# Kernel optimization log

Hardware: AMD Instinct MI355X
Metric: run time of the kernel (lower is better)

## Reference

```python
import jax, jax.numpy as jnp
import numpy as np
from functools import partial

B, T, F = 4096, 256, 32
H1, H2, NT = 64, 32, 3


def _lstm_layer(x, W_ih, W_hh, b_ih, b_hh):
    """Torch-style LSTM (batch_first). x: [B,T,Fin], W_ih: [4H,Fin], W_hh: [4H,H].
    Gate order i, f, g, o. Returns all hidden states [B,T,H]."""
    Bsz = x.shape[0]
    H = W_hh.shape[1]
    # Precompute input contribution for all timesteps (one big GEMM)
    xg = jnp.einsum('btf,gf->btg', x, W_ih) + b_ih + b_hh  # [B,T,4H]

    def step(carry, xg_t):
        h, c = carry
        gates = xg_t + h @ W_hh.T  # [B,4H]
        i, f, g, o = jnp.split(gates, 4, axis=-1)
        i = jax.nn.sigmoid(i)
        f = jax.nn.sigmoid(f)
        g = jnp.tanh(g)
        o = jax.nn.sigmoid(o)
        c = f * c + i * g
        h = o * jnp.tanh(c)
        return (h, c), h

    init = (jnp.zeros((Bsz, H), x.dtype), jnp.zeros((Bsz, H), x.dtype))
    _, hs = jax.lax.scan(step, init, jnp.swapaxes(xg, 0, 1))  # hs: [T,B,H]
    return jnp.swapaxes(hs, 0, 1)


def setup_inputs() -> dict:
    key = jax.random.key(0)
    ks = jax.random.split(key, 12)
    s1 = 1.0 / np.sqrt(H1)
    s2 = 1.0 / np.sqrt(H2)
    u = lambda k, shape, s: jax.random.uniform(k, shape, jnp.float32, -s, s)
    return {
        'x': jax.random.normal(ks[0], (B, T, F), jnp.float32),
        'W_ih1': u(ks[1], (4 * H1, F), s1),
        'W_hh1': u(ks[2], (4 * H1, H1), s1),
        'b_ih1': u(ks[3], (4 * H1,), s1),
        'b_hh1': u(ks[4], (4 * H1,), s1),
        'W_ih2': u(ks[5], (4 * H2, H1), s2),
        'W_hh2': u(ks[6], (4 * H2, H2), s2),
        'b_ih2': u(ks[7], (4 * H2,), s2),
        'b_hh2': u(ks[8], (4 * H2,), s2),
        'W_head': u(ks[9], (NT, H2), s2),
        'b_head': u(ks[10], (NT,), s2),
    }


def reference(x, W_ih1, W_hh1, b_ih1, b_hh1, W_ih2, W_hh2, b_ih2, b_hh2, W_head, b_head):
    h1 = _lstm_layer(x, W_ih1, W_hh1, b_ih1, b_hh1)   # [B,T,64]; dropout is identity in eval
    h2 = _lstm_layer(h1, W_ih2, W_hh2, b_ih2, b_hh2)  # [B,T,32]
    last = h2[:, -1, :]                               # [B,32]
    return last @ W_head.T + b_head                   # [B,3]
```

## Files before the change

kernel.cpp:

```cpp
#include <hip/hip_runtime.h>

#define Bsz 4096
#define Tt  256
#define Ff  32
#define H1  64
#define H2  32
#define NTAPS 3
#define BT  8
#define NTHR 384

typedef _Float16 half8  __attribute__((ext_vector_type(8)));
typedef _Float16 half2v __attribute__((ext_vector_type(2)));
typedef float    f32x4  __attribute__((ext_vector_type(4)));

#define H1S 72
#define XS  40
#define H2S 40
#define HDS 33

__device__ __forceinline__ float lstm_unit(float pi, float pf, float pg, float po,
                                           float& c) {
    const float K1 = 1.4426950408889634f;
    float ei = __builtin_amdgcn_exp2f(-K1 * pi);
    float ef = __builtin_amdgcn_exp2f(-K1 * pf);
    float eg = __builtin_amdgcn_exp2f(-2.0f * K1 * __builtin_fabsf(pg));
    float eo = __builtin_amdgcn_exp2f(-K1 * po);
    float f_ = __builtin_amdgcn_rcpf(1.0f + ef);
    float ig = (1.0f - eg) * __builtin_amdgcn_rcpf((1.0f + ei) * (1.0f + eg));
    ig = __builtin_copysignf(ig, pg);
    c = f_ * c + ig;
    float ec = __builtin_amdgcn_exp2f(-2.0f * K1 * __builtin_fabsf(c));
    float th = (1.0f - ec) * __builtin_amdgcn_rcpf((1.0f + eo) * (1.0f + ec));
    return __builtin_copysignf(th, c);
}

#define MFMA16(a, b, c) __builtin_amdgcn_mfma_f32_16x16x32_f16((a), (b), (c), 0, 0, 0)

__global__ __launch_bounds__(NTHR, 3)
void lstm2_fused(const float* __restrict__ x,
                 const float* __restrict__ Wih1, const float* __restrict__ Whh1,
                 const float* __restrict__ bih1, const float* __restrict__ bhh1,
                 const float* __restrict__ Wih2, const float* __restrict__ Whh2,
                 const float* __restrict__ bih2, const float* __restrict__ bhh2,
                 const float* __restrict__ Whead, const float* __restrict__ bhead,
                 float* __restrict__ out)
{
    __shared__ __align__(16) _Float16 sH1[2][BT][H1S];
    __shared__ __align__(16) _Float16 sX [2][BT][XS];
    __shared__ __align__(16) _Float16 sH2[2][BT][H2S];
    __shared__ __align__(16) float    sHead[BT][HDS];

    const int tid  = threadIdx.x;
    const int wid  = tid >> 6;
    const int lane = tid & 63;
    const int l15  = lane & 15;
    const int q    = lane >> 4;
    const int row8 = l15 & 7;
    const int b0   = blockIdx.x * BT;

    const bool isL1 = (wid < 4);
    const int  hg   = isL1 ? wid : (wid - 4);

    const int r0  = (q >> 1) * 2, r1 = r0 + 1;
    const int bLo = (q & 1) * 4 + (q >> 1) * 2;
    const int col = hg * 16 + l15;

    half8 w[4][3];
    float bias[4];
    if (isL1) {
        #pragma unroll
        for (int G = 0; G < 4; ++G) {
            int gr = G * 64 + hg * 16 + l15;
            #pragma unroll
            for (int c = 0; c < 3; ++c) {
                half8 v;
                #pragma unroll
                for (int e = 0; e < 8; ++e) {
                    int k = c * 32 + q * 8 + e;
                    float f = (k < H1) ? Whh1[gr * H1 + k] : Wih1[gr * Ff + (k - H1)];
                    v[e] = (_Float16)f;
                }
                w[G][c] = v;
            }
            bias[G] = bih1[gr] + bhh1[gr];
        }
    } else {
        #pragma unroll
        for (int G = 0; G < 4; ++G) {
            int gr = G * 32 + hg * 16 + l15;
            #pragma unroll
            for (int c = 0; c < 3; ++c) {
                half8 v;
                #pragma unroll
                for (int e = 0; e < 8; ++e) {
                    int kk = q * 8 + e;
                    float f = (c == 0) ? Whh2[gr * H2 + kk]
                                       : Wih2[gr * H1 + (c - 1) * 32 + kk];
                    v[e] = (_Float16)f;
                }
                w[G][c] = v;
            }
            bias[G] = bih2[gr] + bhh2[gr];
        }
    }

    for (int idx = tid; idx < BT * H1S; idx += NTHR) ((_Float16*)sH1[1])[idx] = (_Float16)0.0f;
    for (int idx = tid; idx < BT * H2S; idx += NTHR) ((_Float16*)sH2[1])[idx] = (_Float16)0.0f;

    float2 rA, rB;
    int xb = 0, xf = 0;
    if (tid >= 256) {
        int t = tid - 256;
        xb = t >> 4; xf = (t & 15) * 2;
        const float* xp = x + ((size_t)(b0 + xb) * Tt) * Ff + xf;
        float2 v0 = *(const float2*)xp;
        half2v h0; h0[0] = (_Float16)v0.x; h0[1] = (_Float16)v0.y;
        *(half2v*)&sX[0][xb][xf] = h0;
        rA = *(const float2*)(xp + 1 * Ff);
        rB = *(const float2*)(xp + 2 * Ff);
    }
    __syncthreads();

    float cs0 = 0.0f, cs1 = 0.0f;

    for (int i = 0; i <= Tt; ++i) {
        const int cur = i & 1, nxt = cur ^ 1;
        const bool active = isL1 ? (i < Tt) : (i >= 1);

        if (active) {
            half8 a0 = *(const half8*)&sH1[nxt][row8][q * 8];
            half8 a1 = *(const half8*)&sH1[nxt][row8][32 + q * 8];
            half8 A0, A1, A2;
            if (isL1) {
                half8 ax = *(const half8*)&sX[cur][row8][q * 8];
                A0 = a0; A1 = a1; A2 = ax;
            } else {
                half8 ah = *(const half8*)&sH2[cur][row8][q * 8];
                A0 = ah; A1 = a0; A2 = a1;
            }
            f32x4 acc[4];
            #pragma unroll
            for (int G = 0; G < 4; ++G) {
                f32x4 a = {bias[G], bias[G], bias[G], bias[G]};
                a = MFMA16(A0, w[G][0], a);
                a = MFMA16(A1, w[G][1], a);
                a = MFMA16(A2, w[G][2], a);
                acc[G] = a;
            }

            float h0 = lstm_unit(acc[0][r0], acc[1][r0], acc[2][r0], acc[3][r0], cs0);
            float h1v = lstm_unit(acc[0][r1], acc[1][r1], acc[2][r1], acc[3][r1], cs1);

            if (isL1) {
                sH1[cur][bLo][col]     = (_Float16)h0;
                sH1[cur][bLo + 1][col] = (_Float16)h1v;
            } else {
                sH2[nxt][bLo][col]     = (_Float16)h0;
                sH2[nxt][bLo + 1][col] = (_Float16)h1v;
                if (i == Tt) { sHead[bLo][col] = h0; sHead[bLo + 1][col] = h1v; }
            }
        }

        if (tid >= 256) {
            if (i + 1 < Tt) {
                half2v hx; hx[0] = (_Float16)rA.x; hx[1] = (_Float16)rA.y;
                *(half2v*)&sX[nxt][xb][xf] = hx;
            }
            rA = rB;
            int tld = (i + 3 < Tt) ? (i + 3) : (Tt - 1);
            rB = *(const float2*)(x + ((size_t)(b0 + xb) * Tt + tld) * Ff + xf);
        }
        __syncthreads();
    }

    if (tid < BT * NTAPS) {
        int b = tid / NTAPS, n = tid - b * NTAPS;
        float s = bhead[n];
        #pragma unroll
        for (int k = 0; k < H2; ++k) s = fmaf(sHead[b][k], Whead[n * H2 + k], s);
        out[(size_t)(b0 + b) * NTAPS + n] = s;
    }
}

extern "C" void kernel_launch(void* const* d_in, const int* in_sizes, int n_in,
                              void* d_out, int out_size, void* d_ws, size_t ws_size,
                              hipStream_t stream) {
    const float* xp    = (const float*)d_in[0];
    const float* Wih1  = (const float*)d_in[1];
    const float* Whh1  = (const float*)d_in[2];
    const float* bih1  = (const float*)d_in[3];
    const float* bhh1  = (const float*)d_in[4];
    const float* Wih2  = (const float*)d_in[5];
    const float* Whh2  = (const float*)d_in[6];
    const float* bih2  = (const float*)d_in[7];
    const float* bhh2  = (const float*)d_in[8];
    const float* Whead = (const float*)d_in[9];
    const float* bhead = (const float*)d_in[10];
    float* outp = (float*)d_out;

    hipLaunchKernelGGL(lstm2_fused, dim3(Bsz / BT), dim3(NTHR), 0, stream,
                       xp, Wih1, Whh1, bih1, bhh1, Wih2, Whh2, bih2, bhh2,
                       Whead, bhead, outp);
}
```

Before: 470.4 us.

## Merge LSTM layers into every wave instead of dedicated per-layer waves

Each block drops from six waves (four for layer 1, two for layer 2) to four, and every wave now computes both layers. Layer-2 work is duplicated across wave pairs at the MFMA level, and each wave evaluates only half of the layer-2 activation rows. The x prefetch is spread across all threads as scalar loads instead of two extra waves doing float2 loads. This removes the imbalance where the layer-2 waves sat idle and shrinks the barrier group. The cost is twice the weight registers per wave, more serial work per wave per step, and fewer blocks resident per CU under the lower launch-bounds occupancy hint.

```diff
diff --git a/kernel.cpp b/kernel.cpp
--- a/kernel.cpp
+++ b/kernel.cpp
@@ -7,10 +7,9 @@
 #define H2  32
 #define NTAPS 3
 #define BT  8
-#define NTHR 384
+#define NTHR 256
 
 typedef _Float16 half8  __attribute__((ext_vector_type(8)));
-typedef _Float16 half2v __attribute__((ext_vector_type(2)));
 typedef float    f32x4  __attribute__((ext_vector_type(4)));
 
 #define H1S 72
@@ -36,7 +35,7 @@
 
 #define MFMA16(a, b, c) __builtin_amdgcn_mfma_f32_16x16x32_f16((a), (b), (c), 0, 0, 0)
 
-__global__ __launch_bounds__(NTHR, 3)
+__global__ __launch_bounds__(NTHR, 2)
 void lstm2_fused(const float* __restrict__ x,
                  const float* __restrict__ Wih1, const float* __restrict__ Whh1,
                  const float* __restrict__ bih1, const float* __restrict__ bhh1,
@@ -58,117 +57,96 @@
     const int row8 = l15 & 7;
     const int b0   = blockIdx.x * BT;
 
-    const bool isL1 = (wid < 4);
-    const int  hg   = isL1 ? wid : (wid - 4);
-
+    const int colL1 = wid * 16 + l15;
     const int r0  = (q >> 1) * 2, r1 = r0 + 1;
     const int bLo = (q & 1) * 4 + (q >> 1) * 2;
-    const int col = hg * 16 + l15;
+    const int hT   = wid >> 1, wpar = wid & 1;
+    const int hL2  = hT * 16 + l15;
+    const int rL2  = 2 * wpar + (q >> 1);
+    const int bL2  = (q & 1) * 4 + 2 * wpar + (q >> 1);
 
-    half8 w[4][3];
-    float bias[4];
-    if (isL1) {
+    half8 w1[4][3], w2[4][3];
+    float bias1[4], bias2[4];
+    #pragma unroll
+    for (int G = 0; G < 4; ++G) {
+        int gr1 = G * 64 + wid * 16 + l15;
+        int gr2 = G * 32 + hT * 16 + l15;
         #pragma unroll
-        for (int G = 0; G < 4; ++G) {
-            int gr = G * 64 + hg * 16 + l15;
+        for (int c = 0; c < 3; ++c) {
+            half8 v1, v2;
             #pragma unroll
-            for (int c = 0; c < 3; ++c) {
-                half8 v;
-                #pragma unroll
-                for (int e = 0; e < 8; ++e) {
-                    int k = c * 32 + q * 8 + e;
-                    float f = (k < H1) ? Whh1[gr * H1 + k] : Wih1[gr * Ff + (k - H1)];
-                    v[e] = (_Float16)f;
-                }
-                w[G][c] = v;
+            for (int e = 0; e < 8; ++e) {
+                int k = c * 32 + q * 8 + e;
+                float f1 = (k < H1) ? Whh1[gr1 * H1 + k] : Wih1[gr1 * Ff + (k - H1)];
+                int kk = q * 8 + e;
+                float f2 = (c == 0) ? Whh2[gr2 * H2 + kk]
+                                    : Wih2[gr2 * H1 + (c - 1) * 32 + kk];
+                v1[e] = (_Float16)f1; v2[e] = (_Float16)f2;
             }
-            bias[G] = bih1[gr] + bhh1[gr];
+            w1[G][c] = v1; w2[G][c] = v2;
         }
-    } else {
-        #pragma unroll
-        for (int G = 0; G < 4; ++G) {
-            int gr = G * 32 + hg * 16 + l15;
-            #pragma unroll
-            for (int c = 0; c < 3; ++c) {
-                half8 v;
-                #pragma unroll
-                for (int e = 0; e < 8; ++e) {
-                    int kk = q * 8 + e;
-                    float f = (c == 0) ? Whh2[gr * H2 + kk]
-                                       : Wih2[gr * H1 + (c - 1) * 32 + kk];
-                    v[e] = (_Float16)f;
-                }
-                w[G][c] = v;
-            }
-            bias[G] = bih2[gr] + bhh2[gr];
-        }
+        bias1[G] = bih1[gr1] + bhh1[gr1];
+        bias2[G] = bih2[gr2] + bhh2[gr2];
     }
 
     for (int idx = tid; idx < BT * H1S; idx += NTHR) ((_Float16*)sH1[1])[idx] = (_Float16)0.0f;
     for (int idx = tid; idx < BT * H2S; idx += NTHR) ((_Float16*)sH2[1])[idx] = (_Float16)0.0f;
 
-    float2 rA, rB;
-    int xb = 0, xf = 0;
-    if (tid >= 256) {
-        int t = tid - 256;
-        xb = t >> 4; xf = (t & 15) * 2;
+    const int xb = tid >> 5, xf = tid & 31;
+    float rA, rB;
+    {
         const float* xp = x + ((size_t)(b0 + xb) * Tt) * Ff + xf;
-        float2 v0 = *(const float2*)xp;
-        half2v h0; h0[0] = (_Float16)v0.x; h0[1] = (_Float16)v0.y;
-        *(half2v*)&sX[0][xb][xf] = h0;
-        rA = *(const float2*)(xp + 1 * Ff);
-        rB = *(const float2*)(xp + 2 * Ff);
+        sX[0][xb][xf] = (_Float16)xp[0];
+        rA = xp[1 * Ff];
+        rB = xp[2 * Ff];
     }
     __syncthreads();
 
-    float cs0 = 0.0f, cs1 = 0.0f;
+    float cs0 = 0.0f, cs1 = 0.0f, cs2 = 0.0f;
 
     for (int i = 0; i <= Tt; ++i) {
         const int cur = i & 1, nxt = cur ^ 1;
-        const bool active = isL1 ? (i < Tt) : (i >= 1);
 
-        if (active) {
-            half8 a0 = *(const half8*)&sH1[nxt][row8][q * 8];
-            half8 a1 = *(const half8*)&sH1[nxt][row8][32 + q * 8];
-            half8 A0, A1, A2;
-            if (isL1) {
-                half8 ax = *(const half8*)&sX[cur][row8][q * 8];
-                A0 = a0; A1 = a1; A2 = ax;
-            } else {
-                half8 ah = *(const half8*)&sH2[cur][row8][q * 8];
-                A0 = ah; A1 = a0; A2 = a1;
-            }
+        half8 a0 = *(const half8*)&sH1[nxt][row8][q * 8];
+        half8 a1 = *(const half8*)&sH1[nxt][row8][32 + q * 8];
+
+        if (i < Tt) {
+            half8 ax = *(const half8*)&sX[cur][row8][q * 8];
             f32x4 acc[4];
             #pragma unroll
             for (int G = 0; G < 4; ++G) {
-                f32x4 a = {bias[G], bias[G], bias[G], bias[G]};
-                a = MFMA16(A0, w[G][0], a);
-                a = MFMA16(A1, w[G][1], a);
-                a = MFMA16(A2, w[G][2], a);
+                f32x4 a = {bias1[G], bias1[G], bias1[G], bias1[G]};
+                a = MFMA16(a0, w1[G][0], a);
+                a = MFMA16(a1, w1[G][1], a);
+                a = MFMA16(ax, w1[G][2], a);
                 acc[G] = a;
             }
-
-            float h0 = lstm_unit(acc[0][r0], acc[1][r0], acc[2][r0], acc[3][r0], cs0);
+            float h0  = lstm_unit(acc[0][r0], acc[1][r0], acc[2][r0], acc[3][r0], cs0);
             float h1v = lstm_unit(acc[0][r1], acc[1][r1], acc[2][r1], acc[3][r1], cs1);
-
-            if (isL1) {
-                sH1[cur][bLo][col]     = (_Float16)h0;
-                sH1[cur][bLo + 1][col] = (_Float16)h1v;
-            } else {
-                sH2[nxt][bLo][col]     = (_Float16)h0;
-                sH2[nxt][bLo + 1][col] = (_Float16)h1v;
-                if (i == Tt) { sHead[bLo][col] = h0; sHead[bLo + 1][col] = h1v; }
+            sH1[cur][bLo][colL1]     = (_Float16)h0;
+            sH1[cur][bLo + 1][colL1] = (_Float16)h1v;
+        }
+        if (i >= 1) {
+            half8 ah = *(const half8*)&sH2[cur][row8][q * 8];
+            f32x4 acc[4];
+            #pragma unroll
+            for (int G = 0; G < 4; ++G) {
+                f32x4 a = {bias2[G], bias2[G], bias2[G], bias2[G]};
+                a = MFMA16(ah, w2[G][0], a);
+                a = MFMA16(a0, w2[G][1], a);
+                a = MFMA16(a1, w2[G][2], a);
+                acc[G] = a;
             }
+            float h2v = lstm_unit(acc[0][rL2], acc[1][rL2], acc[2][rL2], acc[3][rL2], cs2);
+            sH2[nxt][bL2][hL2] = (_Float16)h2v;
+            if (i == Tt) sHead[bL2][hL2] = h2v;
         }
 
-        if (tid >= 256) {
-            if (i + 1 < Tt) {
-                half2v hx; hx[0] = (_Float16)rA.x; hx[1] = (_Float16)rA.y;
-                *(half2v*)&sX[nxt][xb][xf] = hx;
-            }
-            rA = rB;
+        if (i + 1 < Tt) sX[nxt][xb][xf] = (_Float16)rA;
+        rA = rB;
+        {
             int tld = (i + 3 < Tt) ? (i + 3) : (Tt - 1);
-            rB = *(const float2*)(x + ((size_t)(b0 + xb) * Tt + tld) * Ff + xf);
+            rB = x[((size_t)(b0 + xb) * Tt + tld) * Ff + xf];
         }
         __syncthreads();
     }
```

After: 443.7 us. 5.7% less time.
